# Kernel tuning notes

Hardware: AMD Instinct MI355X
Metric: run time of the kernel (lower is better)

The kernel has to match this reference:

```python
import jax, jax.numpy as jnp
import numpy as np

B, C, H, W = 2, 256, 64, 64
D = 4  # max dilation ring


def _offsets():
    offs = [(0, 0)]
    for s in range(1, D + 1):
        for a in (-s, 0, s):
            for b in (-s, 0, s):
                if a != 0 or b != 0:
                    offs.append((a, b))
    return np.array(offs, dtype=np.int32)  # (33, 2)


def setup_inputs() -> dict:
    key = jax.random.key(0)
    k1, k2, k3, k4 = jax.random.split(key, 4)
    scale = 1.0 / np.sqrt(C)
    return {
        "Ft": jax.random.normal(k1, (B, C, H, W), dtype=jnp.float32),
        "Ft_epsilon": jax.random.normal(k2, (B, C, H, W), dtype=jnp.float32),
        "Wf": jax.random.normal(k3, (256, C), dtype=jnp.float32) * scale,
        "bf": jnp.zeros((256,), dtype=jnp.float32),
        "Wg": jax.random.normal(k4, (256, C), dtype=jnp.float32) * scale,
        "bg": jnp.zeros((256,), dtype=jnp.float32),
    }


def reference(Ft, Ft_epsilon, Wf, bf, Wg, bg):
    # 1x1 conv embeddings
    Ef = jnp.einsum("bchw,oc->bohw", Ft, Wf) + bf[None, :, None, None]          # f(Ft)
    Eg = jnp.einsum("bchw,oc->bohw", Ft_epsilon, Wg) + bg[None, :, None, None]  # g(Ft_eps)

    offs = _offsets()                                  # (K,2), K=33
    dx = jnp.asarray(offs[:, 0])[:, None, None]        # (K,1,1)
    dy = jnp.asarray(offs[:, 1])[:, None, None]
    xs = jnp.arange(H)[None, :, None] + dx             # (K,H,1)
    ys = jnp.arange(W)[None, None, :] + dy             # (K,1,W)
    valid = ((xs >= 0) & (xs < H)) & ((ys >= 0) & (ys < W))  # (K,H,W)
    xc = jnp.clip(xs, 0, H - 1)
    yc = jnp.clip(ys, 0, W - 1)

    # gather neighbor embeddings and features: (B,C,K,H,W)
    Ef_n = Ef[:, :, xc, yc]
    Ft_n = Ft[:, :, xc, yc]

    # affinity of center embedding with each neighbor embedding
    aff = jnp.einsum("bchw,bckhw->bkhw", Eg, Ef_n)     # (B,K,H,W)
    aff = jnp.where(valid[None], aff, -jnp.inf)        # clip out-of-bounds neighbors
    w = jax.nn.softmax(aff, axis=1)                    # (B,K,H,W); center always valid

    out = jnp.einsum("bkhw,bckhw->bchw", w, Ft_n)      # (B,C,H,W)
    return out
```

## Files before the change

kernel.cpp:

```cpp
#include <hip/hip_runtime.h>
#include <math.h>

typedef __attribute__((ext_vector_type(4))) float f4;

__device__ __forceinline__ int iclamp(int x, int lo, int hi) { return min(max(x, lo), hi); }

__device__ constexpr int DXC[33] = {0, -1,-1,-1,0,0,1,1,1, -2,-2,-2,0,0,2,2,2, -3,-3,-3,0,0,3,3,3, -4,-4,-4,0,0,4,4,4};
__device__ constexpr int DYC[33] = {0, -1,0,1,-1,1,-1,0,1, -2,0,2,-2,2,-2,0,2, -3,0,3,-3,3,-3,0,3, -4,0,4,-4,4,-4,0,4};

__global__ __launch_bounds__(256, 2) void gemm_f32(
    const float* __restrict__ Wf, const float* __restrict__ bf,
    const float* __restrict__ Wg, const float* __restrict__ bg,
    const float* __restrict__ Ft, const float* __restrict__ FtE,
    float* __restrict__ Ef, float* __restrict__ Eg)
{
    __shared__ float As[2][32][132];
    __shared__ float Bs[2][32][64];

    const int bn = blockIdx.x, bm = blockIdx.y, gb = blockIdx.z;
    const int g = gb >> 1, b = gb & 1;
    const float* Wmat = g ? Wg : Wf;
    const float* bias = g ? bg : bf;
    const float* X = (g ? FtE : Ft) + (size_t)b * 256 * 4096;
    float* E = (g ? Eg : Ef) + (size_t)b * 256 * 4096;

    const int tid = threadIdx.x;
    const int tn = tid & 15, tm = tid >> 4;
    const int m0 = bm * 128, n0 = bn * 64;

    float acc[8][4] = {};
    f4 areg[4], breg[2];

    auto loadA = [&](int kk) {
        #pragma unroll
        for (int i = 0; i < 4; ++i) {
            int f = i * 256 + tid, m = f >> 3, cq = f & 7;
            areg[i] = *(const f4*)&Wmat[(m0 + m) * 256 + kk + cq * 4];
        }
    };
    auto loadB = [&](int kk) {
        #pragma unroll
        for (int i = 0; i < 2; ++i) {
            int f = i * 256 + tid, c = f >> 4, n4 = f & 15;
            breg[i] = *(const f4*)&X[(size_t)(kk + c) * 4096 + n0 + n4 * 4];
        }
    };
    auto storeLDS = [&](int buf) {
        #pragma unroll
        for (int i = 0; i < 4; ++i) {
            int f = i * 256 + tid, m = f >> 3, cq = f & 7;
            As[buf][cq * 4 + 0][m] = areg[i].x;
            As[buf][cq * 4 + 1][m] = areg[i].y;
            As[buf][cq * 4 + 2][m] = areg[i].z;
            As[buf][cq * 4 + 3][m] = areg[i].w;
        }
        #pragma unroll
        for (int i = 0; i < 2; ++i) {
            int f = i * 256 + tid, c = f >> 4, n4 = f & 15;
            *(f4*)&Bs[buf][c][n4 * 4] = breg[i];
        }
    };

    loadA(0); loadB(0); storeLDS(0);
    __syncthreads();

    for (int ch = 0; ch < 8; ++ch) {
        const int buf = ch & 1;
        if (ch < 7) { loadA((ch + 1) * 32); loadB((ch + 1) * 32); }
        #pragma unroll 4
        for (int k = 0; k < 32; ++k) {
            f4 a0 = *(const f4*)&As[buf][k][tm * 8];
            f4 a1 = *(const f4*)&As[buf][k][tm * 8 + 4];
            f4 bb = *(const f4*)&Bs[buf][k][tn * 4];
            #pragma unroll
            for (int ii = 0; ii < 4; ++ii)
                #pragma unroll
                for (int jj = 0; jj < 4; ++jj) {
                    acc[ii][jj]     += a0[ii] * bb[jj];
                    acc[4 + ii][jj] += a1[ii] * bb[jj];
                }
        }
        if (ch < 7) storeLDS(buf ^ 1);
        __syncthreads();
    }

    #pragma unroll
    for (int r = 0; r < 8; ++r) {
        int o = m0 + tm * 8 + r;
        float bvs = bias[o];
        f4 v = { acc[r][0] + bvs, acc[r][1] + bvs, acc[r][2] + bvs, acc[r][3] + bvs };
        *(f4*)&E[(size_t)o * 4096 + n0 + tn * 4] = v;
    }
}

template<int K0, int NK>
__device__ __forceinline__ void aff_accum(const float* __restrict__ base, float* __restrict__ aff)
{
    #pragma unroll
    for (int ch = 0; ch < 8; ++ch) {
        float eg = base[(72 + ch) * 72];
        #pragma unroll
        for (int j = 0; j < NK; ++j) {
            constexpr int kk0 = K0;
            int k = kk0 + j;
            aff[j] += eg * base[((DXC[k] + 4) * 8 + ch) * 72 + DYC[k]];
        }
    }
}

__global__ __launch_bounds__(256, 2) void aff_part(
    const float* __restrict__ Ef, const float* __restrict__ Eg,
    float* __restrict__ part)
{
    __shared__ float L[2][10 * 8 * 72];

    const int h = blockIdx.x, b = blockIdx.y, cseg = blockIdx.z;
    const int tid = threadIdx.x;
    const int w = tid & 63, kg = tid >> 6;
    const size_t plane = (size_t)b * 256 * 4096;
    const float* EfB = Ef + plane;
    const float* EgB = Eg + plane;
    const int cbase = cseg * 64;

    int hr[10];
    #pragma unroll
    for (int d = 0; d < 10; ++d) hr[d] = (d < 9) ? iclamp(h + d - 4, 0, 63) : h;

    f4 vreg[5]; float sreg[3];

    auto load_rnd = [&](int r) {
        const int c0 = cbase + r * 8;
        #pragma unroll
        for (int i = 0; i < 5; ++i) {
            int f = i * 256 + tid, d = f >> 7, rem = f & 127, ch = rem >> 4, c4 = rem & 15;
            const float* src = (d < 9) ? EfB : EgB;
            vreg[i] = *(const f4*)&src[(size_t)(c0 + ch) * 4096 + hr[d] * 64 + c4 * 4];
        }
        #pragma unroll
        for (int i = 0; i < 3; ++i) {
            int e = i * 256 + tid;
            if (e < 640) {
                int row = e >> 3, sc = e & 7, d = row >> 3, ch = row & 7;
                int wsrc = (sc < 4) ? 0 : 63;
                const float* src = (d < 9) ? EfB : EgB;
                sreg[i] = src[(size_t)(c0 + ch) * 4096 + hr[d] * 64 + wsrc];
            }
        }
    };
    auto store_rnd = [&](int buf) {
        float* Lb = L[buf];
        #pragma unroll
        for (int i = 0; i < 5; ++i) {
            int f = i * 256 + tid, d = f >> 7, rem = f & 127, ch = rem >> 4, c4 = rem & 15;
            *(f4*)&Lb[(d * 8 + ch) * 72 + 4 + c4 * 4] = vreg[i];
        }
        #pragma unroll
        for (int i = 0; i < 3; ++i) {
            int e = i * 256 + tid;
            if (e < 640) {
                int row = e >> 3, sc = e & 7, d = row >> 3, ch = row & 7;
                int col = (sc < 4) ? sc : (64 + sc);
                Lb[(d * 8 + ch) * 72 + col] = sreg[i];
            }
        }
    };

    float aff[9] = {0.f,0.f,0.f,0.f,0.f,0.f,0.f,0.f,0.f};

    load_rnd(0); store_rnd(0);
    for (int r = 0; r < 8; ++r) {
        if (r < 7) load_rnd(r + 1);
        __syncthreads();
        const float* base = &L[r & 1][4 + w];
        switch (kg) {
            case 0: aff_accum<0, 9>(base, aff); break;
            case 1: aff_accum<9, 8>(base, aff); break;
            case 2: aff_accum<17, 8>(base, aff); break;
            default: aff_accum<25, 8>(base, aff); break;
        }
        if (r < 7) store_rnd((r + 1) & 1);
    }

    const int k0 = (kg == 0) ? 0 : (kg == 1) ? 9 : (kg == 2) ? 17 : 25;
    const int nk = (kg == 0) ? 9 : 8;
    float* pB = part + (((size_t)cseg * 2 + b) * 33) * 4096 + h * 64 + w;
    for (int j = 0; j < nk; ++j) pB[(size_t)(k0 + j) * 4096] = aff[j];
}

__global__ __launch_bounds__(256, 2) void softmax_k(
    const float* __restrict__ part, float* __restrict__ wgt)
{
    const int id = blockIdx.x * 256 + threadIdx.x;
    const int b = id >> 12, p = id & 4095;
    const int h = p >> 6, w = p & 63;

    float a[33];
    float m = -INFINITY;
    #pragma unroll
    for (int k = 0; k < 33; ++k) {
        float s = part[(((size_t)0 * 2 + b) * 33 + k) * 4096 + p]
                + part[(((size_t)1 * 2 + b) * 33 + k) * 4096 + p]
                + part[(((size_t)2 * 2 + b) * 33 + k) * 4096 + p]
                + part[(((size_t)3 * 2 + b) * 33 + k) * 4096 + p];
        bool valid = ((unsigned)(h + DXC[k]) < 64u) && ((unsigned)(w + DYC[k]) < 64u);
        a[k] = valid ? s : -INFINITY;
        m = fmaxf(m, a[k]);
    }
    float ssum = 0.f;
    #pragma unroll
    for (int k = 0; k < 33; ++k) { float e = __expf(a[k] - m); a[k] = e; ssum += e; }
    float inv = 1.0f / ssum;
    float* wgtB = wgt + (size_t)b * 33 * 4096 + p;
    #pragma unroll
    for (int k = 0; k < 33; ++k) wgtB[(size_t)k * 4096] = a[k] * inv;
}

__global__ __launch_bounds__(256, 2) void out_kernel(
    const float* __restrict__ wgt, const float* __restrict__ Ft,
    float* __restrict__ out)
{
    __shared__ float L[2][9 * 8 * 72];

    const int h = blockIdx.x, b = blockIdx.y, cseg = blockIdx.z;
    const int tid = threadIdx.x;
    const int w = tid & 63, cg = tid >> 6;
    const size_t plane = (size_t)b * 256 * 4096;
    const float* FtB = Ft + plane;
    float* outB = out + plane;
    const int cbase = cseg * 64;
    const int p = h * 64 + w;

    const float* wgtB = wgt + (size_t)b * 33 * 4096 + p;
    float wv[33];
    #pragma unroll
    for (int k = 0; k < 33; ++k) wv[k] = wgtB[(size_t)k * 4096];

    int hr[9];
    #pragma unroll
    for (int d = 0; d < 9; ++d) hr[d] = iclamp(h + d - 4, 0, 63);

    f4 vreg[5]; float sreg[3];

    auto load_rnd = [&](int r) {
        const int c0 = cbase + r * 8;
        #pragma unroll
        for (int i = 0; i < 5; ++i) {
            int f = i * 256 + tid;
            if (f < 1152) {
                int d = f >> 7, rem = f & 127, ch = rem >> 4, c4 = rem & 15;
                vreg[i] = *(const f4*)&FtB[(size_t)(c0 + ch) * 4096 + hr[d] * 64 + c4 * 4];
            }
        }
        #pragma unroll
        for (int i = 0; i < 3; ++i) {
            int e = i * 256 + tid;
            if (e < 576) {
                int row = e >> 3, sc = e & 7, d = row >> 3, ch = row & 7;
                int wsrc = (sc < 4) ? 0 : 63;
                sreg[i] = FtB[(size_t)(c0 + ch) * 4096 + hr[d] * 64 + wsrc];
            }
        }
    };
    auto store_rnd = [&](int buf) {
        float* Lb = L[buf];
        #pragma unroll
        for (int i = 0; i < 5; ++i) {
            int f = i * 256 + tid;
            if (f < 1152) {
                int d = f >> 7, rem = f & 127, ch = rem >> 4, c4 = rem & 15;
                *(f4*)&Lb[(d * 8 + ch) * 72 + 4 + c4 * 4] = vreg[i];
            }
        }
        #pragma unroll
        for (int i = 0; i < 3; ++i) {
            int e = i * 256 + tid;
            if (e < 576) {
                int row = e >> 3, sc = e & 7, d = row >> 3, ch = row & 7;
                int col = (sc < 4) ? sc : (64 + sc);
                Lb[(d * 8 + ch) * 72 + col] = sreg[i];
            }
        }
    };

    load_rnd(0); store_rnd(0);
    for (int r = 0; r < 8; ++r) {
        if (r < 7) load_rnd(r + 1);
        __syncthreads();
        const float* base = &L[r & 1][4 + w];
        #pragma unroll
        for (int u = 0; u < 2; ++u) {
            const float* b2 = base + (cg * 2 + u) * 72;
            float o = 0.f;
            #pragma unroll
            for (int k = 0; k < 33; ++k)
                o += wv[k] * b2[(DXC[k] + 4) * 576 + DYC[k]];
            int c = cbase + r * 8 + cg * 2 + u;
            outB[(size_t)c * 4096 + p] = o;
        }
        if (r < 7) store_rnd((r + 1) & 1);
    }
}

extern "C" void kernel_launch(void* const* d_in, const int* in_sizes, int n_in,
                              void* d_out, int out_size, void* d_ws, size_t ws_size,
                              hipStream_t stream) {
    const float* Ft  = (const float*)d_in[0];
    const float* FtE = (const float*)d_in[1];
    const float* Wf  = (const float*)d_in[2];
    const float* bf  = (const float*)d_in[3];
    const float* Wg  = (const float*)d_in[4];
    const float* bg  = (const float*)d_in[5];
    float* out = (float*)d_out;

    float* Ef  = (float*)d_ws;
    float* Eg  = Ef + (size_t)2 * 256 * 4096;
    float* part = Eg + (size_t)2 * 256 * 4096;
    float* wgt = part + (size_t)4 * 2 * 33 * 4096;

    hipLaunchKernelGGL(gemm_f32, dim3(64, 2, 4), dim3(256), 0, stream,
                       Wf, bf, Wg, bg, Ft, FtE, Ef, Eg);
    hipLaunchKernelGGL(aff_part, dim3(64, 2, 4), dim3(256), 0, stream,
                       Ef, Eg, part);
    hipLaunchKernelGGL(softmax_k, dim3(32), dim3(256), 0, stream,
                       part, wgt);
    hipLaunchKernelGGL(out_kernel, dim3(64, 2, 4), dim3(256), 0, stream,
                       wgt, Ft, out);
}
```

Baseline: 141.4 us.

## Retile GEMM to 128x128 and split channels finer in affinity/output kernels

```diff
diff --git a/kernel.cpp b/kernel.cpp
--- a/kernel.cpp
+++ b/kernel.cpp
@@ -14,10 +14,10 @@
     const float* __restrict__ Ft, const float* __restrict__ FtE,
     float* __restrict__ Ef, float* __restrict__ Eg)
 {
-    __shared__ float As[2][32][132];
-    __shared__ float Bs[2][32][64];
-
-    const int bn = blockIdx.x, bm = blockIdx.y, gb = blockIdx.z;
+    __shared__ float As[2][16][132];
+    __shared__ float Bs[2][16][128];
+
+    const int gb = blockIdx.z;
     const int g = gb >> 1, b = gb & 1;
     const float* Wmat = g ? Wg : Wf;
     const float* bias = g ? bg : bf;
@@ -26,61 +26,55 @@
 
     const int tid = threadIdx.x;
     const int tn = tid & 15, tm = tid >> 4;
-    const int m0 = bm * 128, n0 = bn * 64;
-
-    float acc[8][4] = {};
-    f4 areg[4], breg[2];
-
-    auto loadA = [&](int kk) {
-        #pragma unroll
-        for (int i = 0; i < 4; ++i) {
-            int f = i * 256 + tid, m = f >> 3, cq = f & 7;
-            areg[i] = *(const f4*)&Wmat[(m0 + m) * 256 + kk + cq * 4];
-        }
-    };
-    auto loadB = [&](int kk) {
-        #pragma unroll
-        for (int i = 0; i < 2; ++i) {
-            int f = i * 256 + tid, c = f >> 4, n4 = f & 15;
-            breg[i] = *(const f4*)&X[(size_t)(kk + c) * 4096 + n0 + n4 * 4];
-        }
-    };
-    auto storeLDS = [&](int buf) {
-        #pragma unroll
-        for (int i = 0; i < 4; ++i) {
-            int f = i * 256 + tid, m = f >> 3, cq = f & 7;
-            As[buf][cq * 4 + 0][m] = areg[i].x;
-            As[buf][cq * 4 + 1][m] = areg[i].y;
-            As[buf][cq * 4 + 2][m] = areg[i].z;
-            As[buf][cq * 4 + 3][m] = areg[i].w;
-        }
-        #pragma unroll
-        for (int i = 0; i < 2; ++i) {
-            int f = i * 256 + tid, c = f >> 4, n4 = f & 15;
-            *(f4*)&Bs[buf][c][n4 * 4] = breg[i];
-        }
-    };
-
-    loadA(0); loadB(0); storeLDS(0);
+    const int m0 = blockIdx.y * 128, n0 = blockIdx.x * 128;
+
+    float acc[8][8] = {};
+    f4 areg[2], breg[2];
+
+    auto loadG = [&](int kk) {
+        #pragma unroll
+        for (int i = 0; i < 2; ++i) {
+            int f = i * 256 + tid;
+            areg[i] = *(const f4*)&Wmat[(size_t)(m0 + (f >> 2)) * 256 + kk + (f & 3) * 4];
+            breg[i] = *(const f4*)&X[(size_t)(kk + (f >> 5)) * 4096 + n0 + (f & 31) * 4];
+        }
+    };
+    auto storeL = [&](int buf) {
+        #pragma unroll
+        for (int i = 0; i < 2; ++i) {
+            int f = i * 256 + tid;
+            int o = f >> 2, cq = f & 3;
+            As[buf][cq * 4 + 0][o] = areg[i].x;
+            As[buf][cq * 4 + 1][o] = areg[i].y;
+            As[buf][cq * 4 + 2][o] = areg[i].z;
+            As[buf][cq * 4 + 3][o] = areg[i].w;
+            *(f4*)&Bs[buf][f >> 5][(f & 31) * 4] = breg[i];
+        }
+    };
+
+    loadG(0); storeL(0);
     __syncthreads();
 
-    for (int ch = 0; ch < 8; ++ch) {
+    for (int ch = 0; ch < 16; ++ch) {
         const int buf = ch & 1;
-        if (ch < 7) { loadA((ch + 1) * 32); loadB((ch + 1) * 32); }
-        #pragma unroll 4
-        for (int k = 0; k < 32; ++k) {
+        if (ch < 15) loadG((ch + 1) * 16);
+        #pragma unroll
+        for (int k = 0; k < 16; ++k) {
             f4 a0 = *(const f4*)&As[buf][k][tm * 8];
             f4 a1 = *(const f4*)&As[buf][k][tm * 8 + 4];
-            f4 bb = *(const f4*)&Bs[buf][k][tn * 4];
+            f4 b0 = *(const f4*)&Bs[buf][k][tn * 4];
+            f4 b1 = *(const f4*)&Bs[buf][k][64 + tn * 4];
             #pragma unroll
             for (int ii = 0; ii < 4; ++ii)
                 #pragma unroll
                 for (int jj = 0; jj < 4; ++jj) {
-                    acc[ii][jj]     += a0[ii] * bb[jj];
-                    acc[4 + ii][jj] += a1[ii] * bb[jj];
+                    acc[ii][jj]         += a0[ii] * b0[jj];
+                    acc[ii][4 + jj]     += a0[ii] * b1[jj];
+                    acc[4 + ii][jj]     += a1[ii] * b0[jj];
+                    acc[4 + ii][4 + jj] += a1[ii] * b1[jj];
                 }
         }
-        if (ch < 7) storeLDS(buf ^ 1);
+        if (ch < 15) storeL(buf ^ 1);
         __syncthreads();
     }
 
@@ -88,31 +82,32 @@
     for (int r = 0; r < 8; ++r) {
         int o = m0 + tm * 8 + r;
         float bvs = bias[o];
-        f4 v = { acc[r][0] + bvs, acc[r][1] + bvs, acc[r][2] + bvs, acc[r][3] + bvs };
-        *(f4*)&E[(size_t)o * 4096 + n0 + tn * 4] = v;
+        f4 v0 = { acc[r][0] + bvs, acc[r][1] + bvs, acc[r][2] + bvs, acc[r][3] + bvs };
+        f4 v1 = { acc[r][4] + bvs, acc[r][5] + bvs, acc[r][6] + bvs, acc[r][7] + bvs };
+        *(f4*)&E[(size_t)o * 4096 + n0 + tn * 4] = v0;
+        *(f4*)&E[(size_t)o * 4096 + n0 + 64 + tn * 4] = v1;
     }
 }
 
 template<int K0, int NK>
-__device__ __forceinline__ void aff_accum(const float* __restrict__ base, float* __restrict__ aff)
-{
-    #pragma unroll
-    for (int ch = 0; ch < 8; ++ch) {
-        float eg = base[(72 + ch) * 72];
+__device__ __forceinline__ void aff_acc4(const float* __restrict__ base, float* __restrict__ aff)
+{
+    #pragma unroll
+    for (int ch = 0; ch < 4; ++ch) {
+        float eg = base[(36 + ch) * 72];
         #pragma unroll
         for (int j = 0; j < NK; ++j) {
-            constexpr int kk0 = K0;
-            int k = kk0 + j;
-            aff[j] += eg * base[((DXC[k] + 4) * 8 + ch) * 72 + DYC[k]];
-        }
-    }
-}
-
-__global__ __launch_bounds__(256, 2) void aff_part(
+            int k = K0 + j;
+            aff[j] += eg * base[((DXC[k] + 4) * 4 + ch) * 72 + DYC[k]];
+        }
+    }
+}
+
+__global__ __launch_bounds__(256, 4) void aff_part(
     const float* __restrict__ Ef, const float* __restrict__ Eg,
     float* __restrict__ part)
 {
-    __shared__ float L[2][10 * 8 * 72];
+    __shared__ float L[2][10 * 4 * 72];
 
     const int h = blockIdx.x, b = blockIdx.y, cseg = blockIdx.z;
     const int tid = threadIdx.x;
@@ -120,27 +115,30 @@
     const size_t plane = (size_t)b * 256 * 4096;
     const float* EfB = Ef + plane;
     const float* EgB = Eg + plane;
-    const int cbase = cseg * 64;
+    const int cbase = cseg * 32;
 
     int hr[10];
     #pragma unroll
     for (int d = 0; d < 10; ++d) hr[d] = (d < 9) ? iclamp(h + d - 4, 0, 63) : h;
 
-    f4 vreg[5]; float sreg[3];
+    f4 vreg[3]; float sreg[2];
 
     auto load_rnd = [&](int r) {
-        const int c0 = cbase + r * 8;
-        #pragma unroll
-        for (int i = 0; i < 5; ++i) {
-            int f = i * 256 + tid, d = f >> 7, rem = f & 127, ch = rem >> 4, c4 = rem & 15;
-            const float* src = (d < 9) ? EfB : EgB;
-            vreg[i] = *(const f4*)&src[(size_t)(c0 + ch) * 4096 + hr[d] * 64 + c4 * 4];
-        }
+        const int c0 = cbase + r * 4;
         #pragma unroll
         for (int i = 0; i < 3; ++i) {
+            int f = i * 256 + tid;
+            if (f < 640) {
+                int d = f >> 6, rem = f & 63, ch = rem >> 4, c4 = rem & 15;
+                const float* src = (d < 9) ? EfB : EgB;
+                vreg[i] = *(const f4*)&src[(size_t)(c0 + ch) * 4096 + hr[d] * 64 + c4 * 4];
+            }
+        }
+        #pragma unroll
+        for (int i = 0; i < 2; ++i) {
             int e = i * 256 + tid;
-            if (e < 640) {
-                int row = e >> 3, sc = e & 7, d = row >> 3, ch = row & 7;
+            if (e < 320) {
+                int row = e >> 3, sc = e & 7, d = row >> 2, ch = row & 3;
                 int wsrc = (sc < 4) ? 0 : 63;
                 const float* src = (d < 9) ? EfB : EgB;
                 sreg[i] = src[(size_t)(c0 + ch) * 4096 + hr[d] * 64 + wsrc];
@@ -150,17 +148,20 @@
     auto store_rnd = [&](int buf) {
         float* Lb = L[buf];
         #pragma unroll
-        for (int i = 0; i < 5; ++i) {
-            int f = i * 256 + tid, d = f >> 7, rem = f & 127, ch = rem >> 4, c4 = rem & 15;
-            *(f4*)&Lb[(d * 8 + ch) * 72 + 4 + c4 * 4] = vreg[i];
-        }
-        #pragma unroll
         for (int i = 0; i < 3; ++i) {
+            int f = i * 256 + tid;
+            if (f < 640) {
+                int d = f >> 6, rem = f & 63, ch = rem >> 4, c4 = rem & 15;
+                *(f4*)&Lb[(d * 4 + ch) * 72 + 4 + c4 * 4] = vreg[i];
+            }
+        }
+        #pragma unroll
+        for (int i = 0; i < 2; ++i) {
             int e = i * 256 + tid;
-            if (e < 640) {
-                int row = e >> 3, sc = e & 7, d = row >> 3, ch = row & 7;
+            if (e < 320) {
+                int row = e >> 3, sc = e & 7, d = row >> 2, ch = row & 3;
                 int col = (sc < 4) ? sc : (64 + sc);
-                Lb[(d * 8 + ch) * 72 + col] = sreg[i];
+                Lb[(d * 4 + ch) * 72 + col] = sreg[i];
             }
         }
     };
@@ -173,10 +174,10 @@
         __syncthreads();
         const float* base = &L[r & 1][4 + w];
         switch (kg) {
-            case 0: aff_accum<0, 9>(base, aff); break;
-            case 1: aff_accum<9, 8>(base, aff); break;
-            case 2: aff_accum<17, 8>(base, aff); break;
-            default: aff_accum<25, 8>(base, aff); break;
+            case 0: aff_acc4<0, 9>(base, aff); break;
+            case 1: aff_acc4<9, 8>(base, aff); break;
+            case 2: aff_acc4<17, 8>(base, aff); break;
+            default: aff_acc4<25, 8>(base, aff); break;
         }
         if (r < 7) store_rnd((r + 1) & 1);
     }
@@ -187,10 +188,10 @@
     for (int j = 0; j < nk; ++j) pB[(size_t)(k0 + j) * 4096] = aff[j];
 }
 
-__global__ __launch_bounds__(256, 2) void softmax_k(
+__global__ __launch_bounds__(64) void softmax_k(
     const float* __restrict__ part, float* __restrict__ wgt)
 {
-    const int id = blockIdx.x * 256 + threadIdx.x;
+    const int id = blockIdx.x * 64 + threadIdx.x;
     const int b = id >> 12, p = id & 4095;
     const int h = p >> 6, w = p & 63;
 
@@ -198,10 +199,10 @@
     float m = -INFINITY;
     #pragma unroll
     for (int k = 0; k < 33; ++k) {
-        float s = part[(((size_t)0 * 2 + b) * 33 + k) * 4096 + p]
-                + part[(((size_t)1 * 2 + b) * 33 + k) * 4096 + p]
-                + part[(((size_t)2 * 2 + b) * 33 + k) * 4096 + p]
-                + part[(((size_t)3 * 2 + b) * 33 + k) * 4096 + p];
+        float s = 0.f;
+        #pragma unroll
+        for (int seg = 0; seg < 8; ++seg)
+            s += part[(((size_t)seg * 2 + b) * 33 + k) * 4096 + p];
         bool valid = ((unsigned)(h + DXC[k]) < 64u) && ((unsigned)(w + DYC[k]) < 64u);
         a[k] = valid ? s : -INFINITY;
         m = fmaxf(m, a[k]);
@@ -215,11 +216,11 @@
     for (int k = 0; k < 33; ++k) wgtB[(size_t)k * 4096] = a[k] * inv;
 }
 
-__global__ __launch_bounds__(256, 2) void out_kernel(
+__global__ __launch_bounds__(256, 4) void out_kernel(
     const float* __restrict__ wgt, const float* __restrict__ Ft,
     float* __restrict__ out)
 {
-    __shared__ float L[2][9 * 8 * 72];
+    __shared__ float L[2][9 * 4 * 72];
 
     const int h = blockIdx.x, b = blockIdx.y, cseg = blockIdx.z;
     const int tid = threadIdx.x;
@@ -227,7 +228,7 @@
     const size_t plane = (size_t)b * 256 * 4096;
     const float* FtB = Ft + plane;
     float* outB = out + plane;
-    const int cbase = cseg * 64;
+    const int cbase = cseg * 32;
     const int p = h * 64 + w;
 
     const float* wgtB = wgt + (size_t)b * 33 * 4096 + p;
@@ -239,23 +240,23 @@
     #pragma unroll
     for (int d = 0; d < 9; ++d) hr[d] = iclamp(h + d - 4, 0, 63);
 
-    f4 vreg[5]; float sreg[3];
+    f4 vreg[3]; float sreg[2];
 
     auto load_rnd = [&](int r) {
-        const int c0 = cbase + r * 8;
-        #pragma unroll
-        for (int i = 0; i < 5; ++i) {
-            int f = i * 256 + tid;
-            if (f < 1152) {
-                int d = f >> 7, rem = f & 127, ch = rem >> 4, c4 = rem & 15;
+        const int c0 = cbase + r * 4;
+        #pragma unroll
+        for (int i = 0; i < 3; ++i) {
+            int f = i * 256 + tid;
+            if (f < 576) {
+                int d = f >> 6, rem = f & 63, ch = rem >> 4, c4 = rem & 15;
                 vreg[i] = *(const f4*)&FtB[(size_t)(c0 + ch) * 4096 + hr[d] * 64 + c4 * 4];
             }
         }
         #pragma unroll
-        for (int i = 0; i < 3; ++i) {
+        for (int i = 0; i < 2; ++i) {
             int e = i * 256 + tid;
-            if (e < 576) {
-                int row = e >> 3, sc = e & 7, d = row >> 3, ch = row & 7;
+            if (e < 288) {
+                int row = e >> 3, sc = e & 7, d = row >> 2, ch = row & 3;
                 int wsrc = (sc < 4) ? 0 : 63;
                 sreg[i] = FtB[(size_t)(c0 + ch) * 4096 + hr[d] * 64 + wsrc];
             }
@@ -264,20 +265,20 @@
     auto store_rnd = [&](int buf) {
         float* Lb = L[buf];
         #pragma unroll
-        for (int i = 0; i < 5; ++i) {
-            int f = i * 256 + tid;
-            if (f < 1152) {
-                int d = f >> 7, rem = f & 127, ch = rem >> 4, c4 = rem & 15;
-                *(f4*)&Lb[(d * 8 + ch) * 72 + 4 + c4 * 4] = vreg[i];
-            }
-        }
-        #pragma unroll
         for (int i = 0; i < 3; ++i) {
+            int f = i * 256 + tid;
+            if (f < 576) {
+                int d = f >> 6, rem = f & 63, ch = rem >> 4, c4 = rem & 15;
+                *(f4*)&Lb[(d * 4 + ch) * 72 + 4 + c4 * 4] = vreg[i];
+            }
+        }
+        #pragma unroll
+        for (int i = 0; i < 2; ++i) {
             int e = i * 256 + tid;
-            if (e < 576) {
-                int row = e >> 3, sc = e & 7, d = row >> 3, ch = row & 7;
+            if (e < 288) {
+                int row = e >> 3, sc = e & 7, d = row >> 2, ch = row & 3;
                 int col = (sc < 4) ? sc : (64 + sc);
-                Lb[(d * 8 + ch) * 72 + col] = sreg[i];
+                Lb[(d * 4 + ch) * 72 + col] = sreg[i];
             }
         }
     };
@@ -287,16 +288,12 @@
         if (r < 7) load_rnd(r + 1);
         __syncthreads();
         const float* base = &L[r & 1][4 + w];
-        #pragma unroll
-        for (int u = 0; u < 2; ++u) {
-            const float* b2 = base + (cg * 2 + u) * 72;
-            float o = 0.f;
-            #pragma unroll
-            for (int k = 0; k < 33; ++k)
-                o += wv[k] * b2[(DXC[k] + 4) * 576 + DYC[k]];
-            int c = cbase + r * 8 + cg * 2 + u;
-            outB[(size_t)c * 4096 + p] = o;
-        }
+        float o = 0.f;
+        #pragma unroll
+        for (int k = 0; k < 33; ++k)
+            o += wv[k] * base[((DXC[k] + 4) * 4 + cg) * 72 + DYC[k]];
+        int c = cbase + r * 4 + cg;
+        outB[(size_t)c * 4096 + p] = o;
         if (r < 7) store_rnd((r + 1) & 1);
     }
 }
@@ -315,14 +312,14 @@
     float* Ef  = (float*)d_ws;
     float* Eg  = Ef + (size_t)2 * 256 * 4096;
     float* part = Eg + (size_t)2 * 256 * 4096;
-    float* wgt = part + (size_t)4 * 2 * 33 * 4096;
-
-    hipLaunchKernelGGL(gemm_f32, dim3(64, 2, 4), dim3(256), 0, stream,
+    float* wgt = part + (size_t)8 * 2 * 33 * 4096;
+
+    hipLaunchKernelGGL(gemm_f32, dim3(32, 2, 4), dim3(256), 0, stream,
                        Wf, bf, Wg, bg, Ft, FtE, Ef, Eg);
-    hipLaunchKernelGGL(aff_part, dim3(64, 2, 4), dim3(256), 0, stream,
+    hipLaunchKernelGGL(aff_part, dim3(64, 2, 8), dim3(256), 0, stream,
                        Ef, Eg, part);
-    hipLaunchKernelGGL(softmax_k, dim3(32), dim3(256), 0, stream,
+    hipLaunchKernelGGL(softmax_k, dim3(128), dim3(64), 0, stream,
                        part, wgt);
-    hipLaunchKernelGGL(out_kernel, dim3(64, 2, 4), dim3(256), 0, stream,
+    hipLaunchKernelGGL(out_kernel, dim3(64, 2, 8), dim3(256), 0, stream,
                        wgt, Ft, out);
 }
```

Result: slower. 281.9 us (+99.4%).
